# Optimization experiments

Hardware: AMD Instinct MI355X
Metric: run time of the kernel (lower is better)

The kernel has to match this reference:

```python
import jax, jax.numpy as jnp
import numpy as np


def setup_inputs() -> dict:
    key = jax.random.key(0)
    ks = jax.random.split(key, 6)
    B, T, D, Dg, U = 64, 2048, 256, 256, 256
    return {
        "x": jax.random.normal(ks[0], (B, T, D), dtype=jnp.float32),
        "g": jax.random.normal(ks[1], (B, 1, Dg), dtype=jnp.float32),
        "W": jax.random.normal(ks[2], (D, U), dtype=jnp.float32) * 0.05,
        "Wg": jax.random.normal(ks[3], (Dg, U), dtype=jnp.float32) * 0.05,
        "b": jax.random.normal(ks[4], (U,), dtype=jnp.float32) * 0.05,
        "v": jax.random.normal(ks[5], (U,), dtype=jnp.float32) * 0.05,
    }


def reference(x, g, W, Wg, b, v):
    # x: [B, T, D], g: [B, 1, Dg]
    g2 = g[:, 0, :]                                  # [B, Dg]
    atten_g = (g2 @ Wg)[:, None, :]                  # [B, 1, U]
    # activation is linear (default activation=None in Keras)
    et = jnp.einsum('btd,du->btu', x, W) + atten_g + b   # [B, T, U]
    scores = jnp.einsum('btu,u->bt', et, v)          # [B, T]
    at = jax.nn.softmax(scores, axis=-1)             # softmax over sequence
    return jnp.einsum('bt,btd->bd', at, x)           # weighted sum pooling
```

## Files before the change

### kernel.cpp

```cpp
#include <hip/hip_runtime.h>

#define B 64
#define T 2048
#define D 256
#define U 256
#define NC 16
#define TC (T / NC)

#define WS_WV   0
#define WS_M    (WS_WV + 256)
#define WS_L    (WS_M + B * NC)
#define WS_O    (WS_L + B * NC)

__global__ __launch_bounds__(256) void k_wv(const float* __restrict__ W,
                                            const float* __restrict__ v,
                                            float* __restrict__ wv) {
    int d = threadIdx.x;
    const float4* Wr = (const float4*)(W + d * U);
    const float4* v4 = (const float4*)v;
    float acc = 0.f;
    #pragma unroll 4
    for (int u = 0; u < U / 4; ++u) {
        float4 w = Wr[u];
        float4 vv = v4[u];
        acc += w.x * vv.x + w.y * vv.y + w.z * vv.z + w.w * vv.w;
    }
    wv[d] = acc;
}

__global__ __launch_bounds__(256) void k_fused(const float* __restrict__ x,
                                               const float* __restrict__ wv,
                                               float* __restrict__ pM,
                                               float* __restrict__ pL,
                                               float* __restrict__ pO) {
    int b = blockIdx.x >> 4;
    int c = blockIdx.x & (NC - 1);
    int l = threadIdx.x & 63;
    int q = threadIdx.x >> 6;

    float4 w4 = ((const float4*)wv)[l];
    const float4* xb =
        (const float4*)(x + ((long long)b * T + (long long)c * TC) * D);

    float m = -1e30f, lsum = 0.f;
    float4 acc = {0.f, 0.f, 0.f, 0.f};

    for (int t = q; t < TC; t += 4) {
        float4 xv = xb[(long long)t * 64 + l];
        float s = xv.x * w4.x + xv.y * w4.y + xv.z * w4.z + xv.w * w4.w;
        #pragma unroll
        for (int off = 1; off < 64; off <<= 1)
            s += __shfl_xor(s, off, 64);
        float m_new = fmaxf(m, s);
        float alpha = __expf(m - m_new);
        float p = __expf(s - m_new);
        lsum = lsum * alpha + p;
        acc.x = fmaf(p, xv.x, acc.x * alpha);
        acc.y = fmaf(p, xv.y, acc.y * alpha);
        acc.z = fmaf(p, xv.z, acc.z * alpha);
        acc.w = fmaf(p, xv.w, acc.w * alpha);
        m = m_new;
    }

    __shared__ float4 redO[4][64];
    __shared__ float redM[4], redL[4];
    redO[q][l] = acc;
    if (l == 0) { redM[q] = m; redL[q] = lsum; }
    __syncthreads();
    if (q == 0) {
        float M = fmaxf(fmaxf(redM[0], redM[1]), fmaxf(redM[2], redM[3]));
        float e0 = __expf(redM[0] - M), e1 = __expf(redM[1] - M);
        float e2 = __expf(redM[2] - M), e3 = __expf(redM[3] - M);
        float4 a0 = redO[0][l], a1 = redO[1][l], a2 = redO[2][l], a3 = redO[3][l];
        float4 r;
        r.x = a0.x * e0 + a1.x * e1 + a2.x * e2 + a3.x * e3;
        r.y = a0.y * e0 + a1.y * e1 + a2.y * e2 + a3.y * e3;
        r.z = a0.z * e0 + a1.z * e1 + a2.z * e2 + a3.z * e3;
        r.w = a0.w * e0 + a1.w * e1 + a2.w * e2 + a3.w * e3;
        ((float4*)(pO + (long long)blockIdx.x * D))[l] = r;
        if (l == 0) {
            pM[blockIdx.x] = M;
            pL[blockIdx.x] = redL[0] * e0 + redL[1] * e1 + redL[2] * e2 + redL[3] * e3;
        }
    }
}

__global__ __launch_bounds__(256) void k_combine(const float* __restrict__ pM,
                                                 const float* __restrict__ pL,
                                                 const float* __restrict__ pO,
                                                 float* __restrict__ out) {
    int b = blockIdx.x;
    int d = threadIdx.x;
    float M = -1e30f;
    #pragma unroll
    for (int c = 0; c < NC; ++c)
        M = fmaxf(M, pM[b * NC + c]);
    float denom = 0.f, acc = 0.f;
    #pragma unroll
    for (int c = 0; c < NC; ++c) {
        float e = __expf(pM[b * NC + c] - M);
        denom += e * pL[b * NC + c];
        acc = fmaf(e, pO[((long long)(b * NC + c)) * D + d], acc);
    }
    out[(long long)b * D + d] = acc / denom;
}

extern "C" void kernel_launch(void* const* d_in, const int* in_sizes, int n_in,
                              void* d_out, int out_size, void* d_ws, size_t ws_size,
                              hipStream_t stream) {
    const float* x = (const float*)d_in[0];
    const float* W = (const float*)d_in[2];
    const float* v = (const float*)d_in[5];
    float* ws = (float*)d_ws;
    float* wv = ws + WS_WV;
    float* pM = ws + WS_M;
    float* pL = ws + WS_L;
    float* pO = ws + WS_O;
    float* out = (float*)d_out;

    k_wv<<<1, 256, 0, stream>>>(W, v, wv);
    k_fused<<<B * NC, 256, 0, stream>>>(x, wv, pM, pL, pO);
    k_combine<<<B, 256, 0, stream>>>(pM, pL, pO, out);
}
```

Measured before the change: 211.2 us.

## Fuse split-softmax combine into main kernel via last-block atomic counter

```diff
diff --git a/kernel.cpp b/kernel.cpp
--- a/kernel.cpp
+++ b/kernel.cpp
@@ -4,18 +4,21 @@
 #define T 2048
 #define D 256
 #define U 256
-#define NC 16
+#define NC 32
 #define TC (T / NC)
 
 #define WS_WV   0
-#define WS_M    (WS_WV + 256)
+#define WS_CNT  (WS_WV + 256)
+#define WS_M    (WS_CNT + B)
 #define WS_L    (WS_M + B * NC)
 #define WS_O    (WS_L + B * NC)
 
 __global__ __launch_bounds__(256) void k_wv(const float* __restrict__ W,
                                             const float* __restrict__ v,
-                                            float* __restrict__ wv) {
+                                            float* __restrict__ wv,
+                                            int* __restrict__ cnt) {
     int d = threadIdx.x;
+    if (d < B) cnt[d] = 0;
     const float4* Wr = (const float4*)(W + d * U);
     const float4* v4 = (const float4*)v;
     float acc = 0.f;
@@ -32,8 +35,10 @@
                                                const float* __restrict__ wv,
                                                float* __restrict__ pM,
                                                float* __restrict__ pL,
-                                               float* __restrict__ pO) {
-    int b = blockIdx.x >> 4;
+                                               float* __restrict__ pO,
+                                               int* __restrict__ cnt,
+                                               float* __restrict__ out) {
+    int b = blockIdx.x >> 5;
     int c = blockIdx.x & (NC - 1);
     int l = threadIdx.x & 63;
     int q = threadIdx.x >> 6;
@@ -45,6 +50,7 @@
     float m = -1e30f, lsum = 0.f;
     float4 acc = {0.f, 0.f, 0.f, 0.f};
 
+    #pragma unroll 4
     for (int t = q; t < TC; t += 4) {
         float4 xv = xb[(long long)t * 64 + l];
         float s = xv.x * w4.x + xv.y * w4.y + xv.z * w4.z + xv.w * w4.w;
@@ -64,6 +70,7 @@
 
     __shared__ float4 redO[4][64];
     __shared__ float redM[4], redL[4];
+    __shared__ int isLast;
     redO[q][l] = acc;
     if (l == 0) { redM[q] = m; redL[q] = lsum; }
     __syncthreads();
@@ -83,26 +90,31 @@
             pL[blockIdx.x] = redL[0] * e0 + redL[1] * e1 + redL[2] * e2 + redL[3] * e3;
         }
     }
-}
-
-__global__ __launch_bounds__(256) void k_combine(const float* __restrict__ pM,
-                                                 const float* __restrict__ pL,
-                                                 const float* __restrict__ pO,
-                                                 float* __restrict__ out) {
-    int b = blockIdx.x;
-    int d = threadIdx.x;
-    float M = -1e30f;
-    #pragma unroll
-    for (int c = 0; c < NC; ++c)
-        M = fmaxf(M, pM[b * NC + c]);
-    float denom = 0.f, acc = 0.f;
-    #pragma unroll
-    for (int c = 0; c < NC; ++c) {
-        float e = __expf(pM[b * NC + c] - M);
-        denom += e * pL[b * NC + c];
-        acc = fmaf(e, pO[((long long)(b * NC + c)) * D + d], acc);
+    if (threadIdx.x == 0) {
+        __threadfence();
+        int old = atomicAdd(&cnt[b], 1);
+        isLast = (old == NC - 1);
     }
-    out[(long long)b * D + d] = acc / denom;
+    __syncthreads();
+    if (isLast) {
+        __threadfence();
+        int d = threadIdx.x;
+        volatile const float* vM = pM + b * NC;
+        volatile const float* vL = pL + b * NC;
+        volatile const float* vO = pO + (long long)b * NC * D;
+        float M = -1e30f;
+        #pragma unroll
+        for (int k = 0; k < NC; ++k)
+            M = fmaxf(M, vM[k]);
+        float denom = 0.f, a = 0.f;
+        #pragma unroll
+        for (int k = 0; k < NC; ++k) {
+            float e = __expf(vM[k] - M);
+            denom += e * vL[k];
+            a = fmaf(e, vO[(long long)k * D + d], a);
+        }
+        out[(long long)b * D + d] = a / denom;
+    }
 }
 
 extern "C" void kernel_launch(void* const* d_in, const int* in_sizes, int n_in,
@@ -113,12 +125,12 @@
     const float* v = (const float*)d_in[5];
     float* ws = (float*)d_ws;
     float* wv = ws + WS_WV;
+    int*   cnt = (int*)(ws + WS_CNT);
     float* pM = ws + WS_M;
     float* pL = ws + WS_L;
     float* pO = ws + WS_O;
     float* out = (float*)d_out;
 
-    k_wv<<<1, 256, 0, stream>>>(W, v, wv);
-    k_fused<<<B * NC, 256, 0, stream>>>(x, wv, pM, pL, pO);
-    k_combine<<<B, 256, 0, stream>>>(pM, pL, pO, out);
+    k_wv<<<1, 256, 0, stream>>>(W, v, wv, cnt);
+    k_fused<<<B * NC, 256, 0, stream>>>(x, wv, pM, pL, pO, cnt, out);
 }
```

Result: slower. 314.2 us (+48.8%).

## Load chunk rows into registers up front and use two-pass softmax per wave

Applied to the files above, without the earlier changes.

```diff
diff --git a/kernel.cpp b/kernel.cpp
--- a/kernel.cpp
+++ b/kernel.cpp
@@ -4,8 +4,9 @@
 #define T 2048
 #define D 256
 #define U 256
-#define NC 16
+#define NC 32
 #define TC (T / NC)
+#define RPW 16
 
 #define WS_WV   0
 #define WS_M    (WS_WV + 256)
@@ -33,7 +34,7 @@
                                                float* __restrict__ pM,
                                                float* __restrict__ pL,
                                                float* __restrict__ pO) {
-    int b = blockIdx.x >> 4;
+    int b = blockIdx.x >> 5;
     int c = blockIdx.x & (NC - 1);
     int l = threadIdx.x & 63;
     int q = threadIdx.x >> 6;
@@ -42,24 +43,35 @@
     const float4* xb =
         (const float4*)(x + ((long long)b * T + (long long)c * TC) * D);
 
-    float m = -1e30f, lsum = 0.f;
-    float4 acc = {0.f, 0.f, 0.f, 0.f};
+    float4 xv[RPW];
+    float  s[RPW];
+    #pragma unroll
+    for (int i = 0; i < RPW; ++i)
+        xv[i] = xb[(q * RPW + i) * 64 + l];
 
-    for (int t = q; t < TC; t += 4) {
-        float4 xv = xb[(long long)t * 64 + l];
-        float s = xv.x * w4.x + xv.y * w4.y + xv.z * w4.z + xv.w * w4.w;
+    #pragma unroll
+    for (int i = 0; i < RPW; ++i) {
+        float t = xv[i].x * w4.x + xv[i].y * w4.y + xv[i].z * w4.z + xv[i].w * w4.w;
         #pragma unroll
         for (int off = 1; off < 64; off <<= 1)
-            s += __shfl_xor(s, off, 64);
-        float m_new = fmaxf(m, s);
-        float alpha = __expf(m - m_new);
-        float p = __expf(s - m_new);
-        lsum = lsum * alpha + p;
-        acc.x = fmaf(p, xv.x, acc.x * alpha);
-        acc.y = fmaf(p, xv.y, acc.y * alpha);
-        acc.z = fmaf(p, xv.z, acc.z * alpha);
-        acc.w = fmaf(p, xv.w, acc.w * alpha);
-        m = m_new;
+            t += __shfl_xor(t, off, 64);
+        s[i] = t;
+    }
+
+    float m = s[0];
+    #pragma unroll
+    for (int i = 1; i < RPW; ++i) m = fmaxf(m, s[i]);
+
+    float lsum = 0.f;
+    float4 acc = {0.f, 0.f, 0.f, 0.f};
+    #pragma unroll
+    for (int i = 0; i < RPW; ++i) {
+        float p = __expf(s[i] - m);
+        lsum += p;
+        acc.x = fmaf(p, xv[i].x, acc.x);
+        acc.y = fmaf(p, xv[i].y, acc.y);
+        acc.z = fmaf(p, xv[i].z, acc.z);
+        acc.w = fmaf(p, xv[i].w, acc.w);
     }
 
     __shared__ float4 redO[4][64];
```

Measured after the change: 216.5 us. 1.03x slower.
